# Kernel optimization log

Measured on AMD Instinct MI355X. Metric: run time of the kernel, lower is better.

Reference implementation:

```python
import jax, jax.numpy as jnp
import numpy as np

B, S, H, NH = 2, 2048, 1024, 16
DH = H // NH


def setup_inputs() -> dict:
    key = jax.random.key(0)
    ks = jax.random.split(key, 8)
    scale = 0.02
    return {
        "q": jax.random.normal(ks[0], (B, S, H), dtype=jnp.float32),
        "attention_mask": jax.random.uniform(ks[1], (B, 1, 1, S), dtype=jnp.float32),
        "Wq": jax.random.normal(ks[2], (H, H), dtype=jnp.float32) * scale,
        "bq": jnp.zeros((H,), dtype=jnp.float32),
        "Wk": jax.random.normal(ks[3], (H, H), dtype=jnp.float32) * scale,
        "bk": jnp.zeros((H,), dtype=jnp.float32),
        "Wv": jax.random.normal(ks[4], (H, H), dtype=jnp.float32) * scale,
        "bv": jnp.zeros((H,), dtype=jnp.float32),
    }


def _split_heads(x):
    # [B, S, H] -> [B, NH, S, DH]
    b, s, _ = x.shape
    return x.reshape(b, s, NH, DH).transpose(0, 2, 1, 3)


def reference(q, attention_mask, Wq, bq, Wk, bk, Wv, bv):
    # self-attention: k = v = q
    query = _split_heads(q @ Wq + bq)  # [B, NH, S, DH]
    key = _split_heads(q @ Wk + bk)
    value = _split_heads(q @ Wv + bv)

    scores = jnp.einsum("bhqd,bhkd->bhqk", query, key) / jnp.sqrt(
        jnp.asarray(DH, dtype=query.dtype)
    )
    scores = scores * attention_mask  # multiplicative mask (non-standard)
    attn = jax.nn.softmax(scores, axis=-1)  # dropout off (training=False)
    ctx = jnp.einsum("bhqk,bhkd->bhqd", attn, value)  # [B, NH, S, DH]
    ctx = ctx.transpose(0, 2, 1, 3).reshape(q.shape[0], -1, NH * DH)
    return ctx, attn
```

## Files before the change

kernel.cpp:

```cpp
#include <hip/hip_runtime.h>
#include <hip/hip_bf16.h>

#define B_ 2
#define S_ 2048
#define H_ 1024
#define NH_ 16
#define DH_ 64
#define M_ (B_*S_)
#define N3_ (3*H_)
#define K_ H_

typedef __attribute__((ext_vector_type(8))) short bf16x8;
typedef __attribute__((ext_vector_type(4))) short bf16x4;
typedef __attribute__((ext_vector_type(4))) float f32x4;

__device__ __forceinline__ short f2bf(float f) {
  union { float fv; unsigned u; } v; v.fv = f;
  return (short)((v.u + 0x7FFFu + ((v.u >> 16) & 1u)) >> 16);
}
__device__ __forceinline__ float bf2f(short s) {
  union { unsigned u; float fv; } v; v.u = ((unsigned)(unsigned short)s) << 16;
  return v.fv;
}

#define MFMA16(a,b,c) __builtin_amdgcn_mfma_f32_16x16x32_bf16((a),(b),(c),0,0,0)

__global__ __launch_bounds__(256) void convert_q(const float* __restrict__ q,
                                                 short* __restrict__ qb) {
  int i = blockIdx.x * blockDim.x + threadIdx.x;
  f32x4 v = ((const f32x4*)q)[i];
  bf16x4 o = { f2bf(v[0]), f2bf(v[1]), f2bf(v[2]), f2bf(v[3]) };
  ((bf16x4*)qb)[i] = o;
}

__global__ __launch_bounds__(256) void transpose_w(const float* __restrict__ Wq,
                                                   const float* __restrict__ Wk,
                                                   const float* __restrict__ Wv,
                                                   short* __restrict__ Wt) {
  __shared__ float tile[32][33];
  int w = blockIdx.z;
  const float* W = (w == 0) ? Wq : ((w == 1) ? Wk : Wv);
  int n0 = blockIdx.x * 32, k0 = blockIdx.y * 32;
  int tx = threadIdx.x, ty = threadIdx.y;
  for (int i = 0; i < 4; i++)
    tile[ty + 8*i][tx] = W[(size_t)(k0 + ty + 8*i) * H_ + n0 + tx];
  __syncthreads();
  for (int i = 0; i < 4; i++)
    Wt[(size_t)w * H_ * H_ + (size_t)(n0 + ty + 8*i) * H_ + k0 + tx] =
        f2bf(tile[tx][ty + 8*i]);
}

__global__ __launch_bounds__(256) void qkv_gemm(
    const short* __restrict__ qb,
    const short* __restrict__ Wt,
    const float* __restrict__ bq, const float* __restrict__ bk,
    const float* __restrict__ bv,
    short* __restrict__ Qws, short* __restrict__ Kws, short* __restrict__ VT) {
  __shared__ short Wtile[128 * 32];
  __shared__ short Qtile[128 * 32];

  int bidx = blockIdx.x;
  int mt = bidx & 31, nt = bidx >> 5;
  int t = threadIdx.x;
  int wave = t >> 6, lane = t & 63;
  int g = lane >> 4, l15 = lane & 15;
  int nh = (wave & 1) * 64, mh = (wave >> 1) * 64;
  int mblk = mt * 128, nblk = nt * 128;

  int srow = t >> 2, ssub = t & 3;
  const short* wsrc = Wt + (size_t)(nblk + srow) * K_ + ssub * 8;
  const short* qsrc = qb + (size_t)(mblk + srow) * K_ + ssub * 8;
  short* wdst0 = Wtile + wave * 512;
  short* qdst0 = Qtile + wave * 512;

  f32x4 acc[4][4];
#pragma unroll
  for (int i = 0; i < 4; i++)
#pragma unroll
    for (int j = 0; j < 4; j++) acc[i][j] = (f32x4){0.f,0.f,0.f,0.f};

  for (int k0 = 0; k0 < K_; k0 += 32) {
    __builtin_amdgcn_global_load_lds(wsrc + k0,         wdst0,         16, 0, 0);
    __builtin_amdgcn_global_load_lds(wsrc + 64*K_ + k0, wdst0 + 64*32, 16, 0, 0);
    __builtin_amdgcn_global_load_lds(qsrc + k0,         qdst0,         16, 0, 0);
    __builtin_amdgcn_global_load_lds(qsrc + 64*K_ + k0, qdst0 + 64*32, 16, 0, 0);
    __syncthreads();
    bf16x8 af[4], bfr[4];
#pragma unroll
    for (int tn = 0; tn < 4; tn++)
      af[tn] = *(const bf16x8*)(Wtile + (nh + tn*16 + l15) * 32 + g * 8);
#pragma unroll
    for (int tm = 0; tm < 4; tm++)
      bfr[tm] = *(const bf16x8*)(Qtile + (mh + tm*16 + l15) * 32 + g * 8);
#pragma unroll
    for (int tn = 0; tn < 4; tn++)
#pragma unroll
      for (int tm = 0; tm < 4; tm++)
        acc[tn][tm] = MFMA16(af[tn], bfr[tm], acc[tn][tm]);
    __syncthreads();
  }

  int which = nblk >> 10;
  int cbase = nblk & 1023;
  const float* bias = (which == 0) ? bq : ((which == 1) ? bk : bv);

#pragma unroll
  for (int tm = 0; tm < 4; tm++) {
    int m = mblk + mh + tm*16 + l15;
    int b = m >> 11, s = m & 2047;
#pragma unroll
    for (int tn = 0; tn < 4; tn++) {
      int c = cbase + nh + tn*16 + 4*g;
      int head = c >> 6, d0 = c & 63;
      f32x4 bia = *(const f32x4*)(bias + c);
      short o[4];
#pragma unroll
      for (int r = 0; r < 4; r++) o[r] = f2bf(acc[tn][tm][r] + bia[r]);
      if (which == 2) {
        short* base = VT + ((size_t)(b*NH_ + head) * DH_ + d0) * S_ + s;
#pragma unroll
        for (int r = 0; r < 4; r++) base[(size_t)r * S_] = o[r];
      } else {
        short* dst = ((which == 0) ? Qws : Kws)
                   + ((size_t)(b*NH_ + head) * S_ + s) * DH_ + d0;
        bf16x4 o4 = {o[0], o[1], o[2], o[3]};
        *(bf16x4*)dst = o4;
      }
    }
  }
}

#define STG_K(bufi, kt) do { \
    __builtin_amdgcn_global_load_lds(kSw + (size_t)(kt)*4096,        &Kb[bufi][w*2048],      16, 0, 0); \
    __builtin_amdgcn_global_load_lds(kSw + (size_t)(kt)*4096 + 512,  &Kb[bufi][w*2048+512],  16, 0, 0); \
    __builtin_amdgcn_global_load_lds(kSw + (size_t)(kt)*4096 + 1024, &Kb[bufi][w*2048+1024], 16, 0, 0); \
    __builtin_amdgcn_global_load_lds(kSw + (size_t)(kt)*4096 + 1536, &Kb[bufi][w*2048+1536], 16, 0, 0); \
  } while (0)

__global__ __launch_bounds__(128, 2) void attn_lcalc(
    const short* __restrict__ Qws, const short* __restrict__ Kws,
    const float* __restrict__ mask, float* __restrict__ Linv) {
  __shared__ short Kb[2][4096];
  int bid0 = blockIdx.x;
  int bid = (bid0 & 7) * 128 + (bid0 >> 3);
  int bh = bid >> 5, qt = bid & 31;
  int tid = threadIdx.x;
  int w = tid >> 6, lane = tid & 63;
  int g = lane >> 4, l15 = lane & 15;
  int lr = lane >> 3, l7 = lane & 7;
  int b = bh >> 4;
  int qbase = qt * 64 + w * 32;

  const short* Kh = Kws + (size_t)bh * S_ * DH_;
  const float* mk = mask + b * S_;
  int sw = 8 * (l15 & 7);
  int swc = 8 * (l7 ^ lr);
  const short* kSw = Kh + (size_t)(w*32 + lr) * DH_ + swc;

  const short* qr0 = Qws + (size_t)bh * S_ * DH_ + (size_t)(qbase + l15) * DH_;
  const short* qr1 = qr0 + 16 * DH_;
  bf16x8 q0a = *(const bf16x8*)(qr0 + 8*g), q0b = *(const bf16x8*)(qr0 + 32 + 8*g);
  bf16x8 q1a = *(const bf16x8*)(qr1 + 8*g), q1b = *(const bf16x8*)(qr1 + 32 + 8*g);

  f32x4 ls0 = (f32x4){0.f,0.f,0.f,0.f}, ls1 = (f32x4){0.f,0.f,0.f,0.f};
  STG_K(0, 0);
  __syncthreads();
  int cur = 0;
  for (int kt = 0; kt < 32; kt++) {
    if (kt + 1 < 32) STG_K(cur ^ 1, kt + 1);
    const short* Kt = Kb[cur];
#pragma unroll
    for (int s0i = 0; s0i < 4; s0i++) {
      int s0 = s0i * 16;
      const short* kp = Kt + (s0 + l15) * 64;
      bf16x8 kf0 = *(const bf16x8*)(kp + ((8*g) ^ sw));
      bf16x8 kf1 = *(const bf16x8*)(kp + ((32 + 8*g) ^ sw));
      f32x4 a0 = (f32x4){0.f,0.f,0.f,0.f}, a1 = (f32x4){0.f,0.f,0.f,0.f};
      a0 = MFMA16(kf0, q0a, a0); a0 = MFMA16(kf1, q0b, a0);
      a1 = MFMA16(kf0, q1a, a1); a1 = MFMA16(kf1, q1b, a1);
      f32x4 mv = *(const f32x4*)(mk + kt*64 + s0 + 4*g);
#pragma unroll
      for (int r = 0; r < 4; r++) {
        ls0[r] += __expf(a0[r] * 0.125f * mv[r]);
        ls1[r] += __expf(a1[r] * 0.125f * mv[r]);
      }
    }
    __syncthreads();
    cur ^= 1;
  }
  float l0 = ls0[0]+ls0[1]+ls0[2]+ls0[3];
  float l1 = ls1[0]+ls1[1]+ls1[2]+ls1[3];
  l0 += __shfl_xor(l0, 16); l0 += __shfl_xor(l0, 32);
  l1 += __shfl_xor(l1, 16); l1 += __shfl_xor(l1, 32);
  if (lane < 16) {
    Linv[(size_t)bh * S_ + qbase + lane]      = 1.f / l0;
    Linv[(size_t)bh * S_ + qbase + 16 + lane] = 1.f / l1;
  }
}

#define STG_K4(bufi, kt) do { \
    __builtin_amdgcn_global_load_lds(kS4 + (size_t)(kt)*4096,          &Kb[bufi][w*1024],      16, 0, 0); \
    __builtin_amdgcn_global_load_lds(kS4 + (size_t)(kt)*4096 + 8*DH_,  &Kb[bufi][w*1024+512],  16, 0, 0); \
  } while (0)
#define STG_V4(bufi, kt) do { \
    __builtin_amdgcn_global_load_lds(vS4 + (size_t)(kt)*64,            &Vb[bufi][w*1024],      16, 0, 0); \
    __builtin_amdgcn_global_load_lds(vS4 + (size_t)(kt)*64 + 8*(size_t)S_, &Vb[bufi][w*1024+512], 16, 0, 0); \
  } while (0)

__global__ __launch_bounds__(256, 2) void attn_main(
    const short* __restrict__ Qws, const short* __restrict__ Kws,
    const short* __restrict__ VT, const float* __restrict__ mask,
    const float* __restrict__ Linv,
    float* __restrict__ ctx, float* __restrict__ attn) {
  __shared__ short Kb[2][4096];
  __shared__ short Vb[2][4096];
  __shared__ short Pb[2][64 * 128];
  int bid0 = blockIdx.x;
  int bid = (bid0 & 7) * 128 + (bid0 >> 3);
  int bh = bid >> 5, qt = bid & 31;
  int tid = threadIdx.x;
  int w = tid >> 6, lane = tid & 63;
  int g = lane >> 4, l15 = lane & 15;
  int lhi = lane >> 3, l7 = lane & 7;
  int l31 = lane & 31, lh = lane >> 5;
  int b = bh >> 4, h = bh & 15;
  int qbase = qt * 64 + w * 16;

  const short* Kh = Kws + (size_t)bh * S_ * DH_;
  const short* Vh = VT  + (size_t)bh * DH_ * S_;
  const float* mk = mask + b * S_;
  int sw = 8 * (l15 & 7);
  int swc = 8 * (l7 ^ lhi);
  const short* kS4 = Kh + (size_t)(w*16 + lhi) * DH_ + swc;
  const short* vS4 = Vh + (size_t)(w*16 + lhi) * S_  + swc;

  const short* qr0 = Qws + (size_t)bh * S_ * DH_ + (size_t)(qbase + l15) * DH_;
  bf16x8 q0a = *(const bf16x8*)(qr0 + 8*g), q0b = *(const bf16x8*)(qr0 + 32 + 8*g);
  float linv = Linv[(size_t)bh * S_ + qbase + l15];

  f32x4 oc[4];
#pragma unroll
  for (int tv = 0; tv < 4; tv++) oc[tv] = (f32x4){0.f,0.f,0.f,0.f};

  int prow = w*16 + l15;
  float* ablk = attn + ((size_t)bh * S_ + qt*64) * (size_t)S_;

  STG_K4(0, 0); STG_V4(0, 0);
  __syncthreads();
  int cur = 0;
  for (int kt = 0; kt < 32; kt++) {
    if (kt + 1 < 32) { STG_K4(cur ^ 1, kt + 1); STG_V4(cur ^ 1, kt + 1); }
    if (kt >= 2) {
      int pst = (kt >> 1) - 1;
      const short* Pp = Pb[pst & 1];
      int rbase = w*16 + 8*(kt & 1);
#pragma unroll
      for (int i = 0; i < 4; i++) {
        int row = rbase + 2*i + lh;
        int gi2 = l31 ^ ((row & 7) << 2);
        bf16x4 pv4 = *(const bf16x4*)(&Pp[row*128 + (gi2 << 2)]);
        f32x4 o = { bf2f(pv4[0]), bf2f(pv4[1]), bf2f(pv4[2]), bf2f(pv4[3]) };
        __builtin_nontemporal_store(o,
            (f32x4*)(ablk + (size_t)row * S_ + pst*128 + 4*l31));
      }
    }
    const short* Kt = Kb[cur];
    const short* Vt = Vb[cur];
    short* Pcur = Pb[(kt >> 1) & 1];
#pragma unroll
    for (int khi = 0; khi < 2; khi++) {
      int kh = khi * 32;
      bf16x8 pa;
#pragma unroll
      for (int half = 0; half < 2; half++) {
        int s0 = kh + half * 16;
        const short* kp = Kt + (s0 + l15) * 64;
        bf16x8 kf0 = *(const bf16x8*)(kp + ((8*g) ^ sw));
        bf16x8 kf1 = *(const bf16x8*)(kp + ((32 + 8*g) ^ sw));
        f32x4 a0 = (f32x4){0.f,0.f,0.f,0.f};
        a0 = MFMA16(kf0, q0a, a0); a0 = MFMA16(kf1, q0b, a0);
        f32x4 mv = *(const f32x4*)(mk + kt*64 + s0 + 4*g);
        bf16x4 p4;
#pragma unroll
        for (int r = 0; r < 4; r++) {
          float p = __expf(a0[r] * 0.125f * mv[r]) * linv;
          short pb = f2bf(p);
          p4[r] = pb;
          pa[half*4 + r] = pb;
        }
        int lk = (kt & 1)*64 + s0 + 4*g;
        int gi = (lk >> 2) ^ ((prow & 7) << 2);
        *(bf16x4*)(&Pcur[prow*128 + (gi << 2)]) = p4;
      }
#pragma unroll
      for (int tv = 0; tv < 4; tv++) {
        const short* vp = Vt + (tv*16 + l15) * 64;
        bf16x4 va = *(const bf16x4*)(vp + ((kh + 4*g) ^ sw));
        bf16x4 vb2 = *(const bf16x4*)(vp + ((kh + 16 + 4*g) ^ sw));
        bf16x8 vf = {va[0],va[1],va[2],va[3], vb2[0],vb2[1],vb2[2],vb2[3]};
        oc[tv] = MFMA16(pa, vf, oc[tv]);
      }
    }
    __syncthreads();
    cur ^= 1;
  }

  {
    const short* Pp = Pb[1];
#pragma unroll
    for (int i = 0; i < 8; i++) {
      int row = w*16 + 2*i + lh;
      int gi2 = l31 ^ ((row & 7) << 2);
      bf16x4 pv4 = *(const bf16x4*)(&Pp[row*128 + (gi2 << 2)]);
      f32x4 o = { bf2f(pv4[0]), bf2f(pv4[1]), bf2f(pv4[2]), bf2f(pv4[3]) };
      __builtin_nontemporal_store(o,
          (f32x4*)(ablk + (size_t)row * S_ + 15*128 + 4*l31));
    }
  }

#pragma unroll
  for (int tv = 0; tv < 4; tv++) {
#pragma unroll
    for (int r = 0; r < 4; r++) {
      int q = qbase + 4*g + r;
      ctx[((size_t)b * S_ + q) * H_ + h * DH_ + tv*16 + l15] = oc[tv][r];
    }
  }
}

extern "C" void kernel_launch(void* const* d_in, const int* in_sizes, int n_in,
                              void* d_out, int out_size, void* d_ws, size_t ws_size,
                              hipStream_t stream) {
  const float* q    = (const float*)d_in[0];
  const float* mask = (const float*)d_in[1];
  const float* Wq   = (const float*)d_in[2];
  const float* bq   = (const float*)d_in[3];
  const float* Wk   = (const float*)d_in[4];
  const float* bk   = (const float*)d_in[5];
  const float* Wv   = (const float*)d_in[6];
  const float* bv   = (const float*)d_in[7];

  float* ctx  = (float*)d_out;
  float* attn = ctx + (size_t)B_ * S_ * H_;

  short* qb  = (short*)d_ws;
  short* Wt  = qb  + (size_t)M_ * K_;
  short* Qws = Wt  + (size_t)N3_ * K_;
  short* Kws = Qws + (size_t)B_ * NH_ * S_ * DH_;
  short* VT  = Kws + (size_t)B_ * NH_ * S_ * DH_;
  float* Linv = (float*)(VT + (size_t)B_ * NH_ * S_ * DH_);

  convert_q<<<(M_ * K_) / (256 * 4), 256, 0, stream>>>(q, qb);
  transpose_w<<<dim3(32, 32, 3), dim3(32, 8), 0, stream>>>(Wq, Wk, Wv, Wt);
  qkv_gemm<<<768, 256, 0, stream>>>(qb, Wt, bq, bk, bv, Qws, Kws, VT);
  attn_lcalc<<<1024, 128, 0, stream>>>(Qws, Kws, mask, Linv);
  attn_main<<<1024, 256, 0, stream>>>(Qws, Kws, VT, mask, Linv, ctx, attn);
}
```

Before: 211.3 us.

## Double-buffer QKV GEMM LDS tiles and relax attention-loop wait counts

The QKV projection GEMM now uses two LDS buffers per operand: the async global-to-LDS loads for the next K slice are issued before the MFMAs on the current slice, leaving one barrier per iteration. The goal is to hide global load latency behind matrix work. In the attention loop, the full __syncthreads is replaced by an explicit s_waitcnt vmcnt(4) plus s_barrier on later iterations, so some outstanding memory operations can stay in flight across the barrier. This doubles LDS use in the GEMM, which may reduce occupancy. The partial wait count depends on the exact number of in-flight ops and could be unsafe if that count is wrong.

```diff
diff --git a/kernel.cpp b/kernel.cpp
--- a/kernel.cpp
+++ b/kernel.cpp
@@ -56,8 +56,8 @@
     const float* __restrict__ bq, const float* __restrict__ bk,
     const float* __restrict__ bv,
     short* __restrict__ Qws, short* __restrict__ Kws, short* __restrict__ VT) {
-  __shared__ short Wtile[128 * 32];
-  __shared__ short Qtile[128 * 32];
+  __shared__ short Wtile[2][128 * 32];
+  __shared__ short Qtile[2][128 * 32];
 
   int bidx = blockIdx.x;
   int mt = bidx & 31, nt = bidx >> 5;
@@ -70,8 +70,13 @@
   int srow = t >> 2, ssub = t & 3;
   const short* wsrc = Wt + (size_t)(nblk + srow) * K_ + ssub * 8;
   const short* qsrc = qb + (size_t)(mblk + srow) * K_ + ssub * 8;
-  short* wdst0 = Wtile + wave * 512;
-  short* qdst0 = Qtile + wave * 512;
+
+#define QSTAGE(bufi, k0) do { \
+    __builtin_amdgcn_global_load_lds(wsrc + (k0),         &Wtile[bufi][wave*512],         16, 0, 0); \
+    __builtin_amdgcn_global_load_lds(wsrc + 64*K_ + (k0), &Wtile[bufi][64*32 + wave*512], 16, 0, 0); \
+    __builtin_amdgcn_global_load_lds(qsrc + (k0),         &Qtile[bufi][wave*512],         16, 0, 0); \
+    __builtin_amdgcn_global_load_lds(qsrc + 64*K_ + (k0), &Qtile[bufi][64*32 + wave*512], 16, 0, 0); \
+  } while (0)
 
   f32x4 acc[4][4];
 #pragma unroll
@@ -79,26 +84,27 @@
 #pragma unroll
     for (int j = 0; j < 4; j++) acc[i][j] = (f32x4){0.f,0.f,0.f,0.f};
 
+  QSTAGE(0, 0);
+  __syncthreads();
+  int cur = 0;
   for (int k0 = 0; k0 < K_; k0 += 32) {
-    __builtin_amdgcn_global_load_lds(wsrc + k0,         wdst0,         16, 0, 0);
-    __builtin_amdgcn_global_load_lds(wsrc + 64*K_ + k0, wdst0 + 64*32, 16, 0, 0);
-    __builtin_amdgcn_global_load_lds(qsrc + k0,         qdst0,         16, 0, 0);
-    __builtin_amdgcn_global_load_lds(qsrc + 64*K_ + k0, qdst0 + 64*32, 16, 0, 0);
-    __syncthreads();
+    if (k0 + 32 < K_) QSTAGE(cur ^ 1, k0 + 32);
     bf16x8 af[4], bfr[4];
 #pragma unroll
     for (int tn = 0; tn < 4; tn++)
-      af[tn] = *(const bf16x8*)(Wtile + (nh + tn*16 + l15) * 32 + g * 8);
+      af[tn] = *(const bf16x8*)(&Wtile[cur][(nh + tn*16 + l15) * 32 + g * 8]);
 #pragma unroll
     for (int tm = 0; tm < 4; tm++)
-      bfr[tm] = *(const bf16x8*)(Qtile + (mh + tm*16 + l15) * 32 + g * 8);
+      bfr[tm] = *(const bf16x8*)(&Qtile[cur][(mh + tm*16 + l15) * 32 + g * 8]);
 #pragma unroll
     for (int tn = 0; tn < 4; tn++)
 #pragma unroll
       for (int tm = 0; tm < 4; tm++)
         acc[tn][tm] = MFMA16(af[tn], bfr[tm], acc[tn][tm]);
     __syncthreads();
-  }
+    cur ^= 1;
+  }
+#undef QSTAGE
 
   int which = nblk >> 10;
   int cbase = nblk & 1023;
@@ -301,7 +307,12 @@
         oc[tv] = MFMA16(pa, vf, oc[tv]);
       }
     }
-    __syncthreads();
+    if (kt >= 2) {
+      asm volatile("s_waitcnt vmcnt(4)" ::: "memory");
+    } else {
+      asm volatile("s_waitcnt vmcnt(0)" ::: "memory");
+    }
+    __builtin_amdgcn_s_barrier();
     cur ^= 1;
   }
 
```

After: 218.7 us. +3.5%, slower.

## Enlarge lcalc blocks to share K tiles and shrink P staging buffer

Applied to the files above, without the earlier changes.

attn_lcalc now runs 512 blocks of 256 threads, each covering 128 query rows, so every K tile staged in LDS serves four waves instead of two and global K traffic is halved. attn_main's P staging buffer shrinks from 128 to 64 columns per stage, and the attention-probability rows are written out every iteration instead of every other one. This lowers LDS use so launch bounds can ask for three blocks per CU. The trade-off is smaller, more frequent store batches and more register pressure under the higher occupancy target.

```diff
diff --git a/kernel.cpp b/kernel.cpp
--- a/kernel.cpp
+++ b/kernel.cpp
@@ -130,32 +130,30 @@
   }
 }
 
-#define STG_K(bufi, kt) do { \
-    __builtin_amdgcn_global_load_lds(kSw + (size_t)(kt)*4096,        &Kb[bufi][w*2048],      16, 0, 0); \
-    __builtin_amdgcn_global_load_lds(kSw + (size_t)(kt)*4096 + 512,  &Kb[bufi][w*2048+512],  16, 0, 0); \
-    __builtin_amdgcn_global_load_lds(kSw + (size_t)(kt)*4096 + 1024, &Kb[bufi][w*2048+1024], 16, 0, 0); \
-    __builtin_amdgcn_global_load_lds(kSw + (size_t)(kt)*4096 + 1536, &Kb[bufi][w*2048+1536], 16, 0, 0); \
+#define STG_KL(bufi, kt) do { \
+    __builtin_amdgcn_global_load_lds(kSw + (size_t)(kt)*4096,          &Kb[bufi][w*512],        16, 0, 0); \
+    __builtin_amdgcn_global_load_lds(kSw + (size_t)(kt)*4096 + 32*DH_, &Kb[bufi][2048 + w*512], 16, 0, 0); \
   } while (0)
 
-__global__ __launch_bounds__(128, 2) void attn_lcalc(
+__global__ __launch_bounds__(256) void attn_lcalc(
     const short* __restrict__ Qws, const short* __restrict__ Kws,
     const float* __restrict__ mask, float* __restrict__ Linv) {
   __shared__ short Kb[2][4096];
   int bid0 = blockIdx.x;
-  int bid = (bid0 & 7) * 128 + (bid0 >> 3);
-  int bh = bid >> 5, qt = bid & 31;
+  int bid = (bid0 & 7) * 64 + (bid0 >> 3);
+  int bh = bid >> 4, qt = bid & 15;
   int tid = threadIdx.x;
   int w = tid >> 6, lane = tid & 63;
   int g = lane >> 4, l15 = lane & 15;
   int lr = lane >> 3, l7 = lane & 7;
   int b = bh >> 4;
-  int qbase = qt * 64 + w * 32;
+  int qbase = qt * 128 + w * 32;
 
   const short* Kh = Kws + (size_t)bh * S_ * DH_;
   const float* mk = mask + b * S_;
   int sw = 8 * (l15 & 7);
   int swc = 8 * (l7 ^ lr);
-  const short* kSw = Kh + (size_t)(w*32 + lr) * DH_ + swc;
+  const short* kSw = Kh + (size_t)(w*8 + lr) * DH_ + swc;
 
   const short* qr0 = Qws + (size_t)bh * S_ * DH_ + (size_t)(qbase + l15) * DH_;
   const short* qr1 = qr0 + 16 * DH_;
@@ -163,11 +161,11 @@
   bf16x8 q1a = *(const bf16x8*)(qr1 + 8*g), q1b = *(const bf16x8*)(qr1 + 32 + 8*g);
 
   f32x4 ls0 = (f32x4){0.f,0.f,0.f,0.f}, ls1 = (f32x4){0.f,0.f,0.f,0.f};
-  STG_K(0, 0);
+  STG_KL(0, 0);
   __syncthreads();
   int cur = 0;
   for (int kt = 0; kt < 32; kt++) {
-    if (kt + 1 < 32) STG_K(cur ^ 1, kt + 1);
+    if (kt + 1 < 32) STG_KL(cur ^ 1, kt + 1);
     const short* Kt = Kb[cur];
 #pragma unroll
     for (int s0i = 0; s0i < 4; s0i++) {
@@ -207,14 +205,14 @@
     __builtin_amdgcn_global_load_lds(vS4 + (size_t)(kt)*64 + 8*(size_t)S_, &Vb[bufi][w*1024+512], 16, 0, 0); \
   } while (0)
 
-__global__ __launch_bounds__(256, 2) void attn_main(
+__global__ __launch_bounds__(256, 3) void attn_main(
     const short* __restrict__ Qws, const short* __restrict__ Kws,
     const short* __restrict__ VT, const float* __restrict__ mask,
     const float* __restrict__ Linv,
     float* __restrict__ ctx, float* __restrict__ attn) {
   __shared__ short Kb[2][4096];
   __shared__ short Vb[2][4096];
-  __shared__ short Pb[2][64 * 128];
+  __shared__ short Pb[2][64 * 64];
   int bid0 = blockIdx.x;
   int bid = (bid0 & 7) * 128 + (bid0 >> 3);
   int bh = bid >> 5, qt = bid & 31;
@@ -222,7 +220,6 @@
   int w = tid >> 6, lane = tid & 63;
   int g = lane >> 4, l15 = lane & 15;
   int lhi = lane >> 3, l7 = lane & 7;
-  int l31 = lane & 31, lh = lane >> 5;
   int b = bh >> 4, h = bh & 15;
   int qbase = qt * 64 + w * 16;
 
@@ -250,23 +247,22 @@
   int cur = 0;
   for (int kt = 0; kt < 32; kt++) {
     if (kt + 1 < 32) { STG_K4(cur ^ 1, kt + 1); STG_V4(cur ^ 1, kt + 1); }
-    if (kt >= 2) {
-      int pst = (kt >> 1) - 1;
-      const short* Pp = Pb[pst & 1];
-      int rbase = w*16 + 8*(kt & 1);
+    if (kt >= 1) {
+      const short* Pp = Pb[(kt - 1) & 1];
+      int pk = (kt - 1) * 64;
 #pragma unroll
       for (int i = 0; i < 4; i++) {
-        int row = rbase + 2*i + lh;
-        int gi2 = l31 ^ ((row & 7) << 2);
-        bf16x4 pv4 = *(const bf16x4*)(&Pp[row*128 + (gi2 << 2)]);
+        int row = w*16 + i*4 + (lane >> 4);
+        int gi2 = (lane & 15) ^ ((row & 7) << 1);
+        bf16x4 pv4 = *(const bf16x4*)(&Pp[row*64 + gi2*4]);
         f32x4 o = { bf2f(pv4[0]), bf2f(pv4[1]), bf2f(pv4[2]), bf2f(pv4[3]) };
         __builtin_nontemporal_store(o,
-            (f32x4*)(ablk + (size_t)row * S_ + pst*128 + 4*l31));
+            (f32x4*)(ablk + (size_t)row * S_ + pk + (lane & 15)*4));
       }
     }
     const short* Kt = Kb[cur];
     const short* Vt = Vb[cur];
-    short* Pcur = Pb[(kt >> 1) & 1];
+    short* Pcur = Pb[kt & 1];
 #pragma unroll
     for (int khi = 0; khi < 2; khi++) {
       int kh = khi * 32;
@@ -288,9 +284,9 @@
           p4[r] = pb;
           pa[half*4 + r] = pb;
         }
-        int lk = (kt & 1)*64 + s0 + 4*g;
-        int gi = (lk >> 2) ^ ((prow & 7) << 2);
-        *(bf16x4*)(&Pcur[prow*128 + (gi << 2)]) = p4;
+        int lk = s0 + 4*g;
+        int gi = (lk >> 2) ^ ((prow & 7) << 1);
+        *(bf16x4*)(&Pcur[prow*64 + gi*4]) = p4;
       }
 #pragma unroll
       for (int tv = 0; tv < 4; tv++) {
@@ -308,13 +304,13 @@
   {
     const short* Pp = Pb[1];
 #pragma unroll
-    for (int i = 0; i < 8; i++) {
-      int row = w*16 + 2*i + lh;
-      int gi2 = l31 ^ ((row & 7) << 2);
-      bf16x4 pv4 = *(const bf16x4*)(&Pp[row*128 + (gi2 << 2)]);
+    for (int i = 0; i < 4; i++) {
+      int row = w*16 + i*4 + (lane >> 4);
+      int gi2 = (lane & 15) ^ ((row & 7) << 1);
+      bf16x4 pv4 = *(const bf16x4*)(&Pp[row*64 + gi2*4]);
       f32x4 o = { bf2f(pv4[0]), bf2f(pv4[1]), bf2f(pv4[2]), bf2f(pv4[3]) };
       __builtin_nontemporal_store(o,
-          (f32x4*)(ablk + (size_t)row * S_ + 15*128 + 4*l31));
+          (f32x4*)(ablk + (size_t)row * S_ + 31*64 + (lane & 15)*4));
     }
   }
 
@@ -353,6 +349,6 @@
   convert_q<<<(M_ * K_) / (256 * 4), 256, 0, stream>>>(q, qb);
   transpose_w<<<dim3(32, 32, 3), dim3(32, 8), 0, stream>>>(Wq, Wk, Wv, Wt);
   qkv_gemm<<<768, 256, 0, stream>>>(qb, Wt, bq, bk, bv, Qws, Kws, VT);
-  attn_lcalc<<<1024, 128, 0, stream>>>(Qws, Kws, mask, Linv);
+  attn_lcalc<<<512, 256, 0, stream>>>(Qws, Kws, mask, Linv);
   attn_main<<<1024, 256, 0, stream>>>(Qws, Kws, VT, mask, Linv, ctx, attn);
 }
```

After: 236.2 us. 11.8% more time.

## Fuse softmax denominator pass into main attention kernel

Applied to the files above, without the earlier changes.

Removes the separate attn_lcalc kernel and computes the row-sum of exp(scores*mask) inside the main attention kernel as a first pass over K, before the second pass that writes attn and ctx. This drops one kernel launch and the Linv global round trip. In exchange each wave now handles only 16 query rows during the sum pass, so per-block K traffic and MFMA work for that pass is less efficient than the old 32-row-per-wave layout. The main kernel also gets longer and carries more registers.

```diff
diff --git a/kernel.cpp b/kernel.cpp
--- a/kernel.cpp
+++ b/kernel.cpp
@@ -130,74 +130,6 @@
   }
 }
 
-#define STG_K(bufi, kt) do { \
-    __builtin_amdgcn_global_load_lds(kSw + (size_t)(kt)*4096,        &Kb[bufi][w*2048],      16, 0, 0); \
-    __builtin_amdgcn_global_load_lds(kSw + (size_t)(kt)*4096 + 512,  &Kb[bufi][w*2048+512],  16, 0, 0); \
-    __builtin_amdgcn_global_load_lds(kSw + (size_t)(kt)*4096 + 1024, &Kb[bufi][w*2048+1024], 16, 0, 0); \
-    __builtin_amdgcn_global_load_lds(kSw + (size_t)(kt)*4096 + 1536, &Kb[bufi][w*2048+1536], 16, 0, 0); \
-  } while (0)
-
-__global__ __launch_bounds__(128, 2) void attn_lcalc(
-    const short* __restrict__ Qws, const short* __restrict__ Kws,
-    const float* __restrict__ mask, float* __restrict__ Linv) {
-  __shared__ short Kb[2][4096];
-  int bid0 = blockIdx.x;
-  int bid = (bid0 & 7) * 128 + (bid0 >> 3);
-  int bh = bid >> 5, qt = bid & 31;
-  int tid = threadIdx.x;
-  int w = tid >> 6, lane = tid & 63;
-  int g = lane >> 4, l15 = lane & 15;
-  int lr = lane >> 3, l7 = lane & 7;
-  int b = bh >> 4;
-  int qbase = qt * 64 + w * 32;
-
-  const short* Kh = Kws + (size_t)bh * S_ * DH_;
-  const float* mk = mask + b * S_;
-  int sw = 8 * (l15 & 7);
-  int swc = 8 * (l7 ^ lr);
-  const short* kSw = Kh + (size_t)(w*32 + lr) * DH_ + swc;
-
-  const short* qr0 = Qws + (size_t)bh * S_ * DH_ + (size_t)(qbase + l15) * DH_;
-  const short* qr1 = qr0 + 16 * DH_;
-  bf16x8 q0a = *(const bf16x8*)(qr0 + 8*g), q0b = *(const bf16x8*)(qr0 + 32 + 8*g);
-  bf16x8 q1a = *(const bf16x8*)(qr1 + 8*g), q1b = *(const bf16x8*)(qr1 + 32 + 8*g);
-
-  f32x4 ls0 = (f32x4){0.f,0.f,0.f,0.f}, ls1 = (f32x4){0.f,0.f,0.f,0.f};
-  STG_K(0, 0);
-  __syncthreads();
-  int cur = 0;
-  for (int kt = 0; kt < 32; kt++) {
-    if (kt + 1 < 32) STG_K(cur ^ 1, kt + 1);
-    const short* Kt = Kb[cur];
-#pragma unroll
-    for (int s0i = 0; s0i < 4; s0i++) {
-      int s0 = s0i * 16;
-      const short* kp = Kt + (s0 + l15) * 64;
-      bf16x8 kf0 = *(const bf16x8*)(kp + ((8*g) ^ sw));
-      bf16x8 kf1 = *(const bf16x8*)(kp + ((32 + 8*g) ^ sw));
-      f32x4 a0 = (f32x4){0.f,0.f,0.f,0.f}, a1 = (f32x4){0.f,0.f,0.f,0.f};
-      a0 = MFMA16(kf0, q0a, a0); a0 = MFMA16(kf1, q0b, a0);
-      a1 = MFMA16(kf0, q1a, a1); a1 = MFMA16(kf1, q1b, a1);
-      f32x4 mv = *(const f32x4*)(mk + kt*64 + s0 + 4*g);
-#pragma unroll
-      for (int r = 0; r < 4; r++) {
-        ls0[r] += __expf(a0[r] * 0.125f * mv[r]);
-        ls1[r] += __expf(a1[r] * 0.125f * mv[r]);
-      }
-    }
-    __syncthreads();
-    cur ^= 1;
-  }
-  float l0 = ls0[0]+ls0[1]+ls0[2]+ls0[3];
-  float l1 = ls1[0]+ls1[1]+ls1[2]+ls1[3];
-  l0 += __shfl_xor(l0, 16); l0 += __shfl_xor(l0, 32);
-  l1 += __shfl_xor(l1, 16); l1 += __shfl_xor(l1, 32);
-  if (lane < 16) {
-    Linv[(size_t)bh * S_ + qbase + lane]      = 1.f / l0;
-    Linv[(size_t)bh * S_ + qbase + 16 + lane] = 1.f / l1;
-  }
-}
-
 #define STG_K4(bufi, kt) do { \
     __builtin_amdgcn_global_load_lds(kS4 + (size_t)(kt)*4096,          &Kb[bufi][w*1024],      16, 0, 0); \
     __builtin_amdgcn_global_load_lds(kS4 + (size_t)(kt)*4096 + 8*DH_,  &Kb[bufi][w*1024+512],  16, 0, 0); \
@@ -207,10 +139,9 @@
     __builtin_amdgcn_global_load_lds(vS4 + (size_t)(kt)*64 + 8*(size_t)S_, &Vb[bufi][w*1024+512], 16, 0, 0); \
   } while (0)
 
-__global__ __launch_bounds__(256, 2) void attn_main(
+__global__ __launch_bounds__(256, 2) void attn_fused(
     const short* __restrict__ Qws, const short* __restrict__ Kws,
     const short* __restrict__ VT, const float* __restrict__ mask,
-    const float* __restrict__ Linv,
     float* __restrict__ ctx, float* __restrict__ attn) {
   __shared__ short Kb[2][4096];
   __shared__ short Vb[2][4096];
@@ -236,7 +167,40 @@
 
   const short* qr0 = Qws + (size_t)bh * S_ * DH_ + (size_t)(qbase + l15) * DH_;
   bf16x8 q0a = *(const bf16x8*)(qr0 + 8*g), q0b = *(const bf16x8*)(qr0 + 32 + 8*g);
-  float linv = Linv[(size_t)bh * S_ + qbase + l15];
+
+  f32x4 ls[4];
+#pragma unroll
+  for (int i = 0; i < 4; i++) ls[i] = (f32x4){0.f,0.f,0.f,0.f};
+
+  STG_K4(0, 0);
+  __syncthreads();
+  int cur = 0;
+  for (int kt = 0; kt < 32; kt++) {
+    if (kt + 1 < 32) STG_K4(cur ^ 1, kt + 1);
+    const short* Kt = Kb[cur];
+#pragma unroll
+    for (int s0i = 0; s0i < 4; s0i++) {
+      int s0 = s0i * 16;
+      const short* kp = Kt + (s0 + l15) * 64;
+      bf16x8 kf0 = *(const bf16x8*)(kp + ((8*g) ^ sw));
+      bf16x8 kf1 = *(const bf16x8*)(kp + ((32 + 8*g) ^ sw));
+      f32x4 a0 = (f32x4){0.f,0.f,0.f,0.f};
+      a0 = MFMA16(kf0, q0a, a0); a0 = MFMA16(kf1, q0b, a0);
+      f32x4 mv = *(const f32x4*)(mk + kt*64 + s0 + 4*g);
+#pragma unroll
+      for (int r = 0; r < 4; r++)
+        ls[s0i][r] += __expf(a0[r] * 0.125f * mv[r]);
+    }
+    __syncthreads();
+    cur ^= 1;
+  }
+  float l_lane = (ls[0][0]+ls[0][1]+ls[0][2]+ls[0][3])
+               + (ls[1][0]+ls[1][1]+ls[1][2]+ls[1][3])
+               + (ls[2][0]+ls[2][1]+ls[2][2]+ls[2][3])
+               + (ls[3][0]+ls[3][1]+ls[3][2]+ls[3][3]);
+  l_lane += __shfl_xor(l_lane, 16);
+  l_lane += __shfl_xor(l_lane, 32);
+  float linv = 1.f / l_lane;
 
   f32x4 oc[4];
 #pragma unroll
@@ -247,7 +211,7 @@
 
   STG_K4(0, 0); STG_V4(0, 0);
   __syncthreads();
-  int cur = 0;
+  cur = 0;
   for (int kt = 0; kt < 32; kt++) {
     if (kt + 1 < 32) { STG_K4(cur ^ 1, kt + 1); STG_V4(cur ^ 1, kt + 1); }
     if (kt >= 2) {
@@ -348,11 +312,9 @@
   short* Qws = Wt  + (size_t)N3_ * K_;
   short* Kws = Qws + (size_t)B_ * NH_ * S_ * DH_;
   short* VT  = Kws + (size_t)B_ * NH_ * S_ * DH_;
-  float* Linv = (float*)(VT + (size_t)B_ * NH_ * S_ * DH_);
 
   convert_q<<<(M_ * K_) / (256 * 4), 256, 0, stream>>>(q, qb);
   transpose_w<<<dim3(32, 32, 3), dim3(32, 8), 0, stream>>>(Wq, Wk, Wv, Wt);
   qkv_gemm<<<768, 256, 0, stream>>>(qb, Wt, bq, bk, bv, Qws, Kws, VT);
-  attn_lcalc<<<1024, 128, 0, stream>>>(Qws, Kws, mask, Linv);
-  attn_main<<<1024, 256, 0, stream>>>(Qws, Kws, VT, mask, Linv, ctx, attn);
-}
+  attn_fused<<<1024, 256, 0, stream>>>(Qws, Kws, VT, mask, ctx, attn);
+}
```

Measured after the change: 212.6 us. No clear change (+0.6%).
